# Performance work log

Measured on AMD Instinct MI355X. Metric: run time of the kernel, lower is better.

The kernel has to match this reference:

```python
import jax, jax.numpy as jnp
import numpy as np

EMBED_DIM = 1024
NUM_HEADS = 16
HEAD_DIM = EMBED_DIM // NUM_HEADS
SCALE = HEAD_DIM ** -0.5


def setup_inputs() -> dict:
    key = jax.random.key(0)
    k_x, k_qkv_w, k_qkv_b, k_p_w, k_p_b = jax.random.split(key, 5)
    B, N, C = 4, 2048, EMBED_DIM
    std = C ** -0.5
    return {
        "x": jax.random.normal(k_x, (B, N, C), dtype=jnp.float32),
        "qkv_w": jax.random.normal(k_qkv_w, (C, 3 * C), dtype=jnp.float32) * std,
        "qkv_b": jax.random.normal(k_qkv_b, (3 * C,), dtype=jnp.float32) * 0.02,
        "proj_w": jax.random.normal(k_p_w, (C, C), dtype=jnp.float32) * std,
        "proj_b": jax.random.normal(k_p_b, (C,), dtype=jnp.float32) * 0.02,
    }


def reference(x, qkv_w, qkv_b, proj_w, proj_b):
    B, N, C = x.shape
    H, D = NUM_HEADS, HEAD_DIM
    # fused QKV projection: [B, N, 3C] -> [3, B, H, N, D]
    qkv = (x @ qkv_w + qkv_b).reshape(B, N, 3, H, D).transpose(2, 0, 3, 1, 4)
    q, k, v = qkv[0], qkv[1], qkv[2]
    # explicit N x N attention (faithful to the original, no fused SDPA)
    attn = jnp.einsum("bhqd,bhkd->bhqk", q, k) * SCALE
    attn = jax.nn.softmax(attn, axis=-1)
    out = jnp.einsum("bhqk,bhkd->bhqd", attn, v)  # [B, H, N, D]
    out = out.transpose(0, 2, 1, 3).reshape(B, N, C)
    return out @ proj_w + proj_b
```

## Files before the change

kernel.cpp:

```cpp
#include <hip/hip_runtime.h>
#include <hip/hip_bf16.h>

typedef __bf16 bf16x8 __attribute__((ext_vector_type(8)));
typedef __bf16 bf16x4 __attribute__((ext_vector_type(4)));
typedef float  f32x4  __attribute__((ext_vector_type(4)));

#define MFMA_BF16(a, b, c) __builtin_amdgcn_mfma_f32_16x16x32_bf16((a), (b), (c), 0, 0, 0)

typedef const __attribute__((address_space(1))) void* gas_ptr;
typedef __attribute__((address_space(3))) void* las_ptr;

__device__ __forceinline__ void gload_lds16(const void* g, void* l) {
    __builtin_amdgcn_global_load_lds((gas_ptr)g, (las_ptr)l, 16, 0, 0);
}

#define LOG2E 1.44269504088896f
#define QSCALE 0.1803368801111204f

__global__ __launch_bounds__(256) void cvt_f32_bf16(const float* __restrict__ in,
                                                    __bf16* __restrict__ out, int n4) {
    int i = blockIdx.x * 256 + threadIdx.x;
    if (i < n4) {
        float4 v = ((const float4*)in)[i];
        bf16x4 o = {(__bf16)v.x, (__bf16)v.y, (__bf16)v.z, (__bf16)v.w};
        ((bf16x4*)out)[i] = o;
    }
}

__global__ __launch_bounds__(256) void transpose_cvt(const float* __restrict__ in,
                                                     __bf16* __restrict__ out, int R, int C) {
    __shared__ float t[32][33];
    int bx = blockIdx.x * 32, by = blockIdx.y * 32;
    int x = bx + threadIdx.x;
    for (int j = threadIdx.y; j < 32; j += 8)
        t[j][threadIdx.x] = in[(size_t)(by + j) * C + x];
    __syncthreads();
    int x2 = by + threadIdx.x;
    for (int j = threadIdx.y; j < 32; j += 8)
        out[(size_t)(bx + j) * R + x2] = (__bf16)t[threadIdx.x][j];
}

template <int MODE>
__global__ __launch_bounds__(256) void gemm_bt(const __bf16* __restrict__ A,
                                               const __bf16* __restrict__ Bt,
                                               const float* __restrict__ bias,
                                               float* __restrict__ outp,
                                               __bf16* __restrict__ Qp,
                                               __bf16* __restrict__ Kp,
                                               __bf16* __restrict__ Vp,
                                               int M, int Nn, int K) {
    __shared__ __align__(16) __bf16 As[128 * 32];
    __shared__ __align__(16) __bf16 Bs[128 * 32];
    const int tid = threadIdx.x, lane = tid & 63, w = tid >> 6;
    const int wr = w >> 1, wc = w & 1;
    const int row0 = blockIdx.y * 128, col0 = blockIdx.x * 128;
    const __bf16* Ag = A + (size_t)row0 * K;
    const __bf16* Bg = Bt + (size_t)col0 * K;
    const int lr = lane >> 2;
    const int lk = (lane & 3) * 8;
    const int frow = lane & 15, fq = lane >> 4;
    f32x4 acc[4][4];
    for (int i = 0; i < 4; ++i)
        for (int j = 0; j < 4; ++j) acc[i][j] = (f32x4)0.f;

    for (int k0 = 0; k0 < K; k0 += 32) {
        __syncthreads();
        for (int it = 0; it < 2; ++it) {
            int ci = 2 * w + it;
            gload_lds16(Ag + (size_t)(ci * 16 + lr) * K + k0 + lk, &As[ci * 512]);
            gload_lds16(Bg + (size_t)(ci * 16 + lr) * K + k0 + lk, &Bs[ci * 512]);
        }
        __syncthreads();
        bf16x8 af[4], bf[4];
        for (int i = 0; i < 4; ++i)
            af[i] = *(const bf16x8*)&As[(wr * 64 + i * 16 + frow) * 32 + fq * 8];
        for (int j = 0; j < 4; ++j)
            bf[j] = *(const bf16x8*)&Bs[(wc * 64 + j * 16 + frow) * 32 + fq * 8];
        for (int i = 0; i < 4; ++i)
            for (int j = 0; j < 4; ++j) acc[i][j] = MFMA_BF16(af[i], bf[j], acc[i][j]);
    }

    for (int i = 0; i < 4; ++i) {
        int rbase = row0 + wr * 64 + i * 16 + fq * 4;
        for (int j = 0; j < 4; ++j) {
            int c = col0 + wc * 64 + j * 16 + frow;
            float bv = bias[c];
            if (MODE == 0) {
                int which = c >> 10;
                int h = (c >> 6) & 15;
                int d = c & 63;
                if (which == 2) {
                    int b = rbase >> 11, n = rbase & 2047;
                    bf16x4 vv = {(__bf16)(acc[i][j][0] + bv), (__bf16)(acc[i][j][1] + bv),
                                 (__bf16)(acc[i][j][2] + bv), (__bf16)(acc[i][j][3] + bv)};
                    *(bf16x4*)&Vp[(size_t)(((b << 4) + h) * 64 + d) * 2048 + n] = vv;
                } else {
                    for (int rg = 0; rg < 4; ++rg) {
                        int rr = rbase + rg;
                        int b = rr >> 11, n = rr & 2047;
                        float v = acc[i][j][rg] + bv;
                        if (which == 0)
                            Qp[(size_t)(((b << 4) + h) * 2048 + n) * 64 + d] =
                                (__bf16)(v * QSCALE);
                        else
                            Kp[(size_t)(((b << 4) + h) * 2048 + n) * 64 + d] = (__bf16)v;
                    }
                }
            } else {
                for (int rg = 0; rg < 4; ++rg)
                    outp[(size_t)(rbase + rg) * Nn + c] = acc[i][j][rg] + bv;
            }
        }
    }
}

__global__ __launch_bounds__(256, 4) void flash_attn5(const __bf16* __restrict__ Q,
                                                      const __bf16* __restrict__ K,
                                                      const __bf16* __restrict__ Vt,
                                                      __bf16* __restrict__ O) {
    __shared__ __align__(16) __bf16 Kts[2][4096];
    __shared__ __align__(16) __bf16 Vts[2][4096];
    const int tid = threadIdx.x, lane = tid & 63, w = tid >> 6;
    const int frow = lane & 15, fq = lane >> 4;
    const int bh = blockIdx.y;
    const int q0 = blockIdx.x * 128;
    const __bf16* Qg = Q + ((size_t)bh * 2048 + q0 + w * 32) * 64;
    const __bf16* Kb = K + (size_t)bh * 2048 * 64;
    const __bf16* Vb = Vt + (size_t)bh * 64 * 2048;

    bf16x8 qf[2][2];
#pragma unroll
    for (int nt = 0; nt < 2; ++nt)
#pragma unroll
        for (int ks = 0; ks < 2; ++ks)
            qf[nt][ks] = *(const bf16x8*)(Qg + (nt * 16 + frow) * 64 + ks * 32 + fq * 8);

    bf16x8 ones;
#pragma unroll
    for (int i = 0; i < 8; ++i) ones[i] = (__bf16)1.0f;

    f32x4 acc[2][4];
#pragma unroll
    for (int i = 0; i < 2; ++i)
#pragma unroll
        for (int j = 0; j < 4; ++j) acc[i][j] = (f32x4)0.f;
    f32x4 acc_l[2];
#pragma unroll
    for (int i = 0; i < 2; ++i) acc_l[i] = (f32x4)0.f;

    const int s_r16 = lane >> 2;
    const int s_c8 = (((lane & 3) ^ ((lane >> 3) & 3))) * 8;

    auto stage = [&](int kt, int buf) {
#pragma unroll
        for (int it = 0; it < 2; ++it) {
            int ci = 2 * w + it;
            int ks = ci >> 2;
            int r16 = (ci & 3) * 16 + s_r16;
            gload_lds16(Kb + (size_t)(kt * 64 + r16) * 64 + ks * 32 + s_c8,
                        &Kts[buf][ci * 512]);
            gload_lds16(Vb + (size_t)r16 * 2048 + kt * 64 + ks * 32 + s_c8,
                        &Vts[buf][ci * 512]);
        }
    };

    stage(0, 0);

    const int key = (frow >> 1) & 3;
    const int kslot = (fq ^ key) * 8;
    const int vA = (((fq >> 1) ^ key)) * 8 + (fq & 1) * 4;
    const int vB = ((((fq >> 1) | 2) ^ key)) * 8 + (fq & 1) * 4;

    for (int kt = 0; kt < 32; ++kt) {
        const int cur = kt & 1;
        __syncthreads();
        if (kt < 31) stage(kt + 1, cur ^ 1);

        const __bf16* Kc = Kts[cur];
        const __bf16* Vc = Vts[cur];

#pragma unroll
        for (int ph = 0; ph < 2; ++ph) {
            bf16x8 pf[2];
#pragma unroll
            for (int mi = 0; mi < 2; ++mi) {
                int mt = ph * 2 + mi;
                bf16x8 a0 = *(const bf16x8*)&Kc[(mt * 16 + frow) * 32 + kslot];
                bf16x8 a1 = *(const bf16x8*)&Kc[2048 + (mt * 16 + frow) * 32 + kslot];
#pragma unroll
                for (int nt = 0; nt < 2; ++nt) {
                    f32x4 s = MFMA_BF16(a0, qf[nt][0], (f32x4)0.f);
                    s = MFMA_BF16(a1, qf[nt][1], s);
                    pf[nt][mi * 4 + 0] = (__bf16)__builtin_exp2f(s[0]);
                    pf[nt][mi * 4 + 1] = (__bf16)__builtin_exp2f(s[1]);
                    pf[nt][mi * 4 + 2] = (__bf16)__builtin_exp2f(s[2]);
                    pf[nt][mi * 4 + 3] = (__bf16)__builtin_exp2f(s[3]);
                }
            }

#pragma unroll
            for (int nt = 0; nt < 4; ++nt) {
                const __bf16* vrow = &Vc[ph * 2048 + (nt * 16 + frow) * 32];
                bf16x4 lo = *(const bf16x4*)&vrow[vA];
                bf16x4 hi = *(const bf16x4*)&vrow[vB];
                bf16x8 vf;
                vf[0] = lo[0]; vf[1] = lo[1]; vf[2] = lo[2]; vf[3] = lo[3];
                vf[4] = hi[0]; vf[5] = hi[1]; vf[6] = hi[2]; vf[7] = hi[3];
#pragma unroll
                for (int mq = 0; mq < 2; ++mq)
                    acc[mq][nt] = MFMA_BF16(pf[mq], vf, acc[mq][nt]);
            }
#pragma unroll
            for (int mq = 0; mq < 2; ++mq)
                acc_l[mq] = MFMA_BF16(pf[mq], ones, acc_l[mq]);
        }
    }

    const int b = bh >> 4, h = bh & 15;
#pragma unroll
    for (int mq = 0; mq < 2; ++mq)
#pragma unroll
        for (int r = 0; r < 4; ++r) {
            float linv = 1.0f / acc_l[mq][r];
            int qg = q0 + w * 32 + mq * 16 + fq * 4 + r;
            __bf16* orow = O + ((size_t)(b * 2048 + qg)) * 1024 + h * 64 + frow;
#pragma unroll
            for (int nt = 0; nt < 4; ++nt)
                orow[nt * 16] = (__bf16)(acc[mq][nt][r] * linv);
        }
}

extern "C" void kernel_launch(void* const* d_in, const int* in_sizes, int n_in,
                              void* d_out, int out_size, void* d_ws, size_t ws_size,
                              hipStream_t stream) {
    const float* x      = (const float*)d_in[0];
    const float* qkv_w  = (const float*)d_in[1];
    const float* qkv_b  = (const float*)d_in[2];
    const float* proj_w = (const float*)d_in[3];
    const float* proj_b = (const float*)d_in[4];
    float* out = (float*)d_out;

    char* ws = (char*)d_ws;
    __bf16* Xb     = (__bf16*)(ws);
    __bf16* Wqkvt  = (__bf16*)(ws + 16777216);
    __bf16* Wpt    = (__bf16*)(ws + 23068672);
    __bf16* Qb     = (__bf16*)(ws + 25165824);
    __bf16* Kb     = (__bf16*)(ws + 41943040);
    __bf16* Vtb    = (__bf16*)(ws + 58720256);
    __bf16* AttnOut = Xb;

    cvt_f32_bf16<<<8192, 256, 0, stream>>>(x, Xb, 2097152);
    transpose_cvt<<<dim3(96, 32), dim3(32, 8), 0, stream>>>(qkv_w, Wqkvt, 1024, 3072);
    transpose_cvt<<<dim3(32, 32), dim3(32, 8), 0, stream>>>(proj_w, Wpt, 1024, 1024);

    gemm_bt<0><<<dim3(24, 64), 256, 0, stream>>>(Xb, Wqkvt, qkv_b, nullptr,
                                                 Qb, Kb, Vtb, 8192, 3072, 1024);

    flash_attn5<<<dim3(16, 64), 256, 0, stream>>>(Qb, Kb, Vtb, AttnOut);

    gemm_bt<1><<<dim3(8, 64), 256, 0, stream>>>(AttnOut, Wpt, proj_b, out,
                                                nullptr, nullptr, nullptr, 8192, 1024, 1024);
}
```

Before: 313.0 us.

## Remap workgroups per XCD, permute V layout for single loads, unroll double buffer

Both GEMMs and the attention kernel now launch a 1D grid and remap block IDs so that consecutive tiles share an XCD (id&7 striding), which should improve L2 reuse of shared K/V and weight tiles. The QKV GEMM epilogue writes V with a permuted key index so the attention kernel can read each V fragment with one 16-byte LDS load instead of two 8-byte loads plus repacking. The attention loop is unrolled by two with fixed buffer pointers, and s_setprio raises wave priority around the PV MFMA block. The V permutation must stay exactly matched to the P fragment ordering, or the results will be wrong.

```diff
diff --git a/kernel.cpp b/kernel.cpp
--- a/kernel.cpp
+++ b/kernel.cpp
@@ -53,7 +53,12 @@
     __shared__ __align__(16) __bf16 Bs[128 * 32];
     const int tid = threadIdx.x, lane = tid & 63, w = tid >> 6;
     const int wr = w >> 1, wc = w & 1;
-    const int row0 = blockIdx.y * 128, col0 = blockIdx.x * 128;
+    const int nbx = Nn >> 7;
+    const int nwg = (M >> 7) * nbx;
+    const int cpx = nwg >> 3;
+    const int id = blockIdx.x;
+    const int nid = (id & 7) * cpx + (id >> 3);
+    const int row0 = (nid / nbx) * 128, col0 = (nid % nbx) * 128;
     const __bf16* Ag = A + (size_t)row0 * K;
     const __bf16* Bg = Bt + (size_t)col0 * K;
     const int lr = lane >> 2;
@@ -91,9 +96,11 @@
                 int d = c & 63;
                 if (which == 2) {
                     int b = rbase >> 11, n = rbase & 2047;
+                    int nph = (n & ~31) | (((n >> 2) & 3) << 3) | (((n >> 4) & 1) << 2) |
+                              (n & 3);
                     bf16x4 vv = {(__bf16)(acc[i][j][0] + bv), (__bf16)(acc[i][j][1] + bv),
                                  (__bf16)(acc[i][j][2] + bv), (__bf16)(acc[i][j][3] + bv)};
-                    *(bf16x4*)&Vp[(size_t)(((b << 4) + h) * 64 + d) * 2048 + n] = vv;
+                    *(bf16x4*)&Vp[(size_t)(((b << 4) + h) * 64 + d) * 2048 + nph] = vv;
                 } else {
                     for (int rg = 0; rg < 4; ++rg) {
                         int rr = rbase + rg;
@@ -114,7 +121,7 @@
     }
 }
 
-__global__ __launch_bounds__(256, 4) void flash_attn5(const __bf16* __restrict__ Q,
+__global__ __launch_bounds__(256, 4) void flash_attn6(const __bf16* __restrict__ Q,
                                                       const __bf16* __restrict__ K,
                                                       const __bf16* __restrict__ Vt,
                                                       __bf16* __restrict__ O) {
@@ -122,8 +129,10 @@
     __shared__ __align__(16) __bf16 Vts[2][4096];
     const int tid = threadIdx.x, lane = tid & 63, w = tid >> 6;
     const int frow = lane & 15, fq = lane >> 4;
-    const int bh = blockIdx.y;
-    const int q0 = blockIdx.x * 128;
+    const int id = blockIdx.x;
+    const int nid = (id & 7) * 128 + (id >> 3);
+    const int bh = nid >> 4;
+    const int q0 = (nid & 15) * 128;
     const __bf16* Qg = Q + ((size_t)bh * 2048 + q0 + w * 32) * 64;
     const __bf16* Kb = K + (size_t)bh * 2048 * 64;
     const __bf16* Vb = Vt + (size_t)bh * 64 * 2048;
@@ -151,33 +160,25 @@
     const int s_r16 = lane >> 2;
     const int s_c8 = (((lane & 3) ^ ((lane >> 3) & 3))) * 8;
 
-    auto stage = [&](int kt, int buf) {
+    auto stage = [&](int kt, __bf16* Kd, __bf16* Vd) {
 #pragma unroll
         for (int it = 0; it < 2; ++it) {
             int ci = 2 * w + it;
             int ks = ci >> 2;
             int r16 = (ci & 3) * 16 + s_r16;
-            gload_lds16(Kb + (size_t)(kt * 64 + r16) * 64 + ks * 32 + s_c8,
-                        &Kts[buf][ci * 512]);
-            gload_lds16(Vb + (size_t)r16 * 2048 + kt * 64 + ks * 32 + s_c8,
-                        &Vts[buf][ci * 512]);
+            gload_lds16(Kb + (size_t)(kt * 64 + r16) * 64 + ks * 32 + s_c8, Kd + ci * 512);
+            gload_lds16(Vb + (size_t)r16 * 2048 + kt * 64 + ks * 32 + s_c8, Vd + ci * 512);
         }
     };
 
-    stage(0, 0);
+    stage(0, Kts[0], Vts[0]);
 
     const int key = (frow >> 1) & 3;
-    const int kslot = (fq ^ key) * 8;
-    const int vA = (((fq >> 1) ^ key)) * 8 + (fq & 1) * 4;
-    const int vB = ((((fq >> 1) | 2) ^ key)) * 8 + (fq & 1) * 4;
-
-    for (int kt = 0; kt < 32; ++kt) {
-        const int cur = kt & 1;
+    const int slot = (fq ^ key) * 8;
+
+    auto body = [&](int kt, const __bf16* Kc, const __bf16* Vc, __bf16* Kn, __bf16* Vn) {
         __syncthreads();
-        if (kt < 31) stage(kt + 1, cur ^ 1);
-
-        const __bf16* Kc = Kts[cur];
-        const __bf16* Vc = Vts[cur];
+        if (kt < 31) stage(kt + 1, Kn, Vn);
 
 #pragma unroll
         for (int ph = 0; ph < 2; ++ph) {
@@ -185,8 +186,8 @@
 #pragma unroll
             for (int mi = 0; mi < 2; ++mi) {
                 int mt = ph * 2 + mi;
-                bf16x8 a0 = *(const bf16x8*)&Kc[(mt * 16 + frow) * 32 + kslot];
-                bf16x8 a1 = *(const bf16x8*)&Kc[2048 + (mt * 16 + frow) * 32 + kslot];
+                bf16x8 a0 = *(const bf16x8*)&Kc[(mt * 16 + frow) * 32 + slot];
+                bf16x8 a1 = *(const bf16x8*)&Kc[2048 + (mt * 16 + frow) * 32 + slot];
 #pragma unroll
                 for (int nt = 0; nt < 2; ++nt) {
                     f32x4 s = MFMA_BF16(a0, qf[nt][0], (f32x4)0.f);
@@ -198,22 +199,22 @@
                 }
             }
 
+            __builtin_amdgcn_s_setprio(1);
 #pragma unroll
             for (int nt = 0; nt < 4; ++nt) {
-                const __bf16* vrow = &Vc[ph * 2048 + (nt * 16 + frow) * 32];
-                bf16x4 lo = *(const bf16x4*)&vrow[vA];
-                bf16x4 hi = *(const bf16x4*)&vrow[vB];
-                bf16x8 vf;
-                vf[0] = lo[0]; vf[1] = lo[1]; vf[2] = lo[2]; vf[3] = lo[3];
-                vf[4] = hi[0]; vf[5] = hi[1]; vf[6] = hi[2]; vf[7] = hi[3];
-#pragma unroll
-                for (int mq = 0; mq < 2; ++mq)
-                    acc[mq][nt] = MFMA_BF16(pf[mq], vf, acc[mq][nt]);
+                bf16x8 vf = *(const bf16x8*)&Vc[ph * 2048 + (nt * 16 + frow) * 32 + slot];
+                acc[0][nt] = MFMA_BF16(pf[0], vf, acc[0][nt]);
+                acc[1][nt] = MFMA_BF16(pf[1], vf, acc[1][nt]);
             }
-#pragma unroll
-            for (int mq = 0; mq < 2; ++mq)
-                acc_l[mq] = MFMA_BF16(pf[mq], ones, acc_l[mq]);
-        }
+            acc_l[0] = MFMA_BF16(pf[0], ones, acc_l[0]);
+            acc_l[1] = MFMA_BF16(pf[1], ones, acc_l[1]);
+            __builtin_amdgcn_s_setprio(0);
+        }
+    };
+
+    for (int kt = 0; kt < 32; kt += 2) {
+        body(kt, Kts[0], Vts[0], Kts[1], Vts[1]);
+        body(kt + 1, Kts[1], Vts[1], Kts[0], Vts[0]);
     }
 
     const int b = bh >> 4, h = bh & 15;
@@ -253,11 +254,11 @@
     transpose_cvt<<<dim3(96, 32), dim3(32, 8), 0, stream>>>(qkv_w, Wqkvt, 1024, 3072);
     transpose_cvt<<<dim3(32, 32), dim3(32, 8), 0, stream>>>(proj_w, Wpt, 1024, 1024);
 
-    gemm_bt<0><<<dim3(24, 64), 256, 0, stream>>>(Xb, Wqkvt, qkv_b, nullptr,
-                                                 Qb, Kb, Vtb, 8192, 3072, 1024);
-
-    flash_attn5<<<dim3(16, 64), 256, 0, stream>>>(Qb, Kb, Vtb, AttnOut);
-
-    gemm_bt<1><<<dim3(8, 64), 256, 0, stream>>>(AttnOut, Wpt, proj_b, out,
-                                                nullptr, nullptr, nullptr, 8192, 1024, 1024);
-}
+    gemm_bt<0><<<1536, 256, 0, stream>>>(Xb, Wqkvt, qkv_b, nullptr,
+                                         Qb, Kb, Vtb, 8192, 3072, 1024);
+
+    flash_attn6<<<1024, 256, 0, stream>>>(Qb, Kb, Vtb, AttnOut);
+
+    gemm_bt<1><<<512, 256, 0, stream>>>(AttnOut, Wpt, proj_b, out,
+                                        nullptr, nullptr, nullptr, 8192, 1024, 1024);
+}
```

Result: faster. 302.3 us (-3.4%).
